# Performance work log

Measured on AMD Instinct MI355X. Metric: run time of the kernel, lower is better.

Reference implementation:

```python
import jax, jax.numpy as jnp
import numpy as np

K = 3
STRIDE = 1
PAD = 1


def setup_inputs() -> dict:
    key = jax.random.key(0)
    k1, k2, k3 = jax.random.split(key, 3)
    N, C, H, W = 4, 256, 64, 64
    outC = 256
    x = jax.random.normal(k1, (N, C, H, W), dtype=jnp.float32)
    # offset/mask conv params (torch inits these to 0; small random makes the test nontrivial)
    conv_offset_w = jax.random.normal(k2, (3 * K * K, C, K, K), dtype=jnp.float32) * 0.01
    conv_offset_b = jnp.zeros((3 * K * K,), dtype=jnp.float32)
    # xavier-normal scale for dcn weight
    fan = C * K * K + outC * K * K
    dcn_weight = jax.random.normal(k3, (outC, C, K, K), dtype=jnp.float32) * np.float32(np.sqrt(2.0 / fan))
    return {"x": x, "conv_offset_w": conv_offset_w, "conv_offset_b": conv_offset_b, "dcn_weight": dcn_weight}


def _dcn(x, w_off, b_off, dcn_weight):
    k, s, p = K, STRIDE, PAD
    N, C, H, W = x.shape
    outC = dcn_weight.shape[0]
    KK = k * k
    # offset/mask prediction conv
    om = jax.lax.conv_general_dilated(
        x, w_off, (s, s), [(p, p), (p, p)],
        dimension_numbers=("NCHW", "OIHW", "NCHW")) + b_off[None, :, None, None]
    offset = om[:, : 2 * KK]
    mask = jax.nn.sigmoid(om[:, 2 * KK:])
    oH = (H + 2 * p - (k - 1)) // s
    oW = (W + 2 * p - (k - 1)) // s
    # pad with an extra row/col at bottom-right so floor+1 indexing is in-bounds (as in torch code)
    px = jnp.pad(x, ((0, 0), (0, 0), (p, p + 1), (p, p + 1)))
    px = jnp.transpose(px, (0, 2, 3, 1))  # (N, H+2p+1, W+2p+1, C)
    offset = jnp.transpose(offset, (0, 2, 3, 1)).reshape(N, oH, oW, KK, 2)  # (...,(y,x))
    mask = jnp.transpose(mask, (0, 2, 3, 1))  # (N, oH, oW, KK)
    base_y = jnp.arange(oH, dtype=jnp.float32) * s + p
    base_x = jnp.arange(oW, dtype=jnp.float32) * s + p
    half = (k - 1) // 2
    inner_y = jnp.repeat(jnp.arange(k, dtype=jnp.float32) - half, k)  # kernel-tap y offsets
    inner_x = jnp.tile(jnp.arange(k, dtype=jnp.float32) - half, k)   # kernel-tap x offsets
    pos_y = base_y[None, :, None, None] + inner_y[None, None, None, :] + offset[..., 0]
    pos_x = base_x[None, None, :, None] + inner_x[None, None, None, :] + offset[..., 1]
    pos_y = jnp.clip(pos_y, 0.0, H + 2 * p - 1.0)
    pos_x = jnp.clip(pos_x, 0.0, W + 2 * p - 1.0)
    y1 = jnp.floor(pos_y)
    x1 = jnp.floor(pos_x)
    y1i = y1.astype(jnp.int32)
    x1i = x1.astype(jnp.int32)
    nidx = jnp.arange(N)[:, None, None, None]
    # bilinear gathers: each (N, oH, oW, KK, C)
    v1 = px[nidx, y1i, x1i]
    v2 = px[nidx, y1i, x1i + 1]
    v3 = px[nidx, y1i + 1, x1i]
    v4 = px[nidx, y1i + 1, x1i + 1]
    lh = (pos_y - y1)[..., None]
    lw = (pos_x - x1)[..., None]
    hh = 1.0 - lh
    hw = 1.0 - lw
    value = hh * hw * v1 + hh * lw * v2 + lh * hw * v3 + lh * lw * v4
    value = value * mask[..., None]  # modulated
    w = dcn_weight.reshape(outC, C, KK)
    # sum over in_C and kernel taps -> NCHW output
    out = jnp.einsum("nhwkc,ock->nohw", value, w)
    return out


def reference(x, conv_offset_w, conv_offset_b, dcn_weight):
    return _dcn(x, conv_offset_w, conv_offset_b, dcn_weight)
```

## Files before the change

kernel.cpp:

```cpp
#include <hip/hip_runtime.h>
#include <type_traits>


typedef __bf16 bf16x8 __attribute__((ext_vector_type(8)));
typedef float  f32x4  __attribute__((ext_vector_type(4)));
typedef unsigned short ushort8 __attribute__((ext_vector_type(8)));
typedef unsigned int   uint4v  __attribute__((ext_vector_type(4)));

#define XBF_OFF   0u
#define WREP_OFF  8388608u
#define WMAIN_OFF 8536064u
#define OM_OFF    9715712u

#define LGKM0_BAR() do { __builtin_amdgcn_s_waitcnt(0xC07F); __builtin_amdgcn_s_barrier(); } while (0)

template <int N> using ic = std::integral_constant<int, N>;

__device__ __forceinline__ unsigned short f2bf(float f) {
  unsigned int u = __float_as_uint(f);
  u += 0x7fffu + ((u >> 16) & 1u);
  return (unsigned short)(u >> 16);
}
__device__ __forceinline__ float bf2f(unsigned short h) {
  return __uint_as_float(((unsigned int)h) << 16);
}

__global__ __launch_bounds__(256) void k_pre(const float* __restrict__ x,
                                             const float* __restrict__ w_off,
                                             const float* __restrict__ dcn_w,
                                             unsigned short* __restrict__ xbf,
                                             unsigned short* __restrict__ wrep,
                                             unsigned short* __restrict__ wmain) {
  __shared__ float tile[32][65];
  __shared__ unsigned short lsh[2304];
  int b = blockIdx.x;
  int t = threadIdx.x;
  if (b < 2048) {
    int n  = b >> 9;
    int cb = (b >> 6) & 7;
    int xb = b & 63;
    int xx  = t & 63;
    int cc0 = t >> 6;
#pragma unroll
    for (int j = 0; j < 8; ++j) {
      int cc = cc0 + j * 4;
      tile[cc][xx] = x[((size_t)(n * 256 + cb * 32 + cc) << 12) + xb * 64 + xx];
    }
    __syncthreads();
    int ccw = t & 31;
    int xw0 = t >> 5;
#pragma unroll
    for (int j = 0; j < 8; ++j) {
      int xw = xw0 + j * 8;
      xbf[((size_t)((n << 12) + xb * 64 + xw)) * 256 + cb * 32 + ccw] = f2bf(tile[ccw][xw]);
    }
  } else {
    int ocb = b - 2048;
    const float* src;
    unsigned short* dst;
    int oc;
    if (ocb < 32) { oc = ocb; src = w_off; dst = wrep; }
    else          { oc = ocb - 32; src = dcn_w; dst = wmain; }
    if (ocb < 32 && oc >= 27) {
#pragma unroll
      for (int j = 0; j < 9; ++j) dst[oc * 2304 + j * 256 + t] = 0;
      return;
    }
    const float* base = src + (size_t)oc * 2304;
#pragma unroll
    for (int j = 0; j < 9; ++j) lsh[j * 256 + t] = f2bf(base[t * 9 + j]);
    __syncthreads();
#pragma unroll
    for (int j = 0; j < 9; ++j) dst[oc * 2304 + j * 256 + t] = lsh[j * 256 + t];
  }
}

__global__ __launch_bounds__(1024) void k_offconv(const unsigned short* __restrict__ xbf,
                                                  const unsigned short* __restrict__ wrep,
                                                  const float* __restrict__ bias,
                                                  float* __restrict__ om) {
  __shared__ __align__(16) unsigned short SHa[4][64 * 64];
  __shared__ __align__(16) unsigned short SHb[4][32 * 64];
  int t = threadIdx.x;
  int wave = t >> 6, lane = t & 63;
  int grp = wave >> 2, wv = wave & 3;
  int tg = t & 255;
  int bm = ((blockIdx.x & 7) << 5) + (blockIdx.x >> 3);
  int n = bm >> 6, oy = bm & 63;

  unsigned short* As = SHa[grp];
  unsigned short* Bs = SHb[grp];

  int arow = tg >> 2, acc4 = tg & 3;
  int brow = tg >> 3, bch = tg & 7;

  f32x4 acc0 = {0.f, 0.f, 0.f, 0.f};
  f32x4 acc1 = {0.f, 0.f, 0.f, 0.f};

  ushort8 av[2][2]; ushort8 bv[2];
  auto prefetch = [&](int ktg, auto slotc) {
    constexpr int slot = decltype(slotc)::value;
    int kk = ktg >> 2;
    int c0 = (ktg & 3) * 64;
    int dy = kk / 3 - 1, dx = kk % 3 - 1;
    int yy = oy + dy, xxg = arow + dx;
    bool ok = ((unsigned)yy < 64u) && ((unsigned)xxg < 64u);
    const unsigned short* p = xbf + (size_t)(((n * 64 + yy) * 64 + xxg) * 256 + c0 + acc4 * 16);
#pragma unroll
    for (int g = 0; g < 2; ++g)
      av[slot][g] = ok ? *(const ushort8*)(p + g * 8) : (ushort8){0,0,0,0,0,0,0,0};
    bv[slot] = *(const ushort8*)(wrep + (size_t)brow * 2304 + ktg * 64 + bch * 8);
  };

  int k0 = grp * 9;
  prefetch(k0, ic<0>{});
  prefetch(k0 + 1, ic<1>{});
  int mr = lane & 15, q = lane >> 4;

  auto step = [&](int kt, auto slotc) {
    constexpr int slot = decltype(slotc)::value;
    LGKM0_BAR();
#pragma unroll
    for (int g = 0; g < 2; ++g) {
      int ch = (acc4 * 2 + g) ^ (arow & 7);
      *(ushort8*)&As[arow * 64 + ch * 8] = av[slot][g];
    }
    { int ch = bch ^ (brow & 7);
      *(ushort8*)&Bs[brow * 64 + ch * 8] = bv[slot]; }
    if (kt + 2 < 9) prefetch(k0 + kt + 2, slotc);
    LGKM0_BAR();
#pragma unroll
    for (int kh = 0; kh < 2; ++kh) {
      int coff = ((q + kh * 4) ^ (mr & 7)) * 8;
      bf16x8 a  = *(const bf16x8*)&As[(wv * 16 + mr) * 64 + coff];
      bf16x8 b0 = *(const bf16x8*)&Bs[mr * 64 + coff];
      bf16x8 b1 = *(const bf16x8*)&Bs[(16 + mr) * 64 + coff];
      acc0 = __builtin_amdgcn_mfma_f32_16x16x32_bf16(a, b0, acc0, 0, 0, 0);
      acc1 = __builtin_amdgcn_mfma_f32_16x16x32_bf16(a, b1, acc1, 0, 0, 0);
    }
  };
  for (int kp = 0; kp < 4; ++kp) {
    step(2 * kp, ic<0>{});
    step(2 * kp + 1, ic<1>{});
  }
  step(8, ic<0>{});

  float* scratch = (float*)&SHa[0][0];
  __syncthreads();
  if (grp > 0) {
#pragma unroll
    for (int nt = 0; nt < 2; ++nt) {
      f32x4 a = nt ? acc1 : acc0;
#pragma unroll
      for (int rg = 0; rg < 4; ++rg)
        scratch[(grp - 1) * 2048 + (wv * 16 + q * 4 + rg) * 32 + nt * 16 + mr] = a[rg];
    }
  }
  __syncthreads();
  if (grp == 0) {
    int r0 = bm * 64;
#pragma unroll
    for (int nt = 0; nt < 2; ++nt) {
      f32x4 a = nt ? acc1 : acc0;
      int oc = nt * 16 + mr;
      float bvl = (oc < 27) ? bias[oc] : 0.f;
#pragma unroll
      for (int rg = 0; rg < 4; ++rg) {
        int pl = wv * 16 + q * 4 + rg;
        float v = a[rg] + bvl + scratch[pl * 32 + oc] +
                  scratch[2048 + pl * 32 + oc] + scratch[4096 + pl * 32 + oc];
        if (oc >= 18 && oc < 27) v = 1.f / (1.f + __expf(-v));
        om[(r0 + pl) * 32 + oc] = v;
      }
    }
  }
}

__global__ __launch_bounds__(1024) void k_gemm_fused(const unsigned short* __restrict__ xbf,
                                                     const float* __restrict__ om,
                                                     const unsigned short* __restrict__ wB,
                                                     float* __restrict__ out) {
  __shared__ __align__(16) unsigned short Ab[3][128 * 64];
  __shared__ __align__(16) unsigned short Bb[3][128 * 64];
  int t = threadIdx.x;
  int wave = t >> 6, lane = t & 63;
  int wm = wave & 3, wn = wave >> 2;
  int bmx = ((blockIdx.x & 7) << 4) + (blockIdx.x >> 3);
  int r0 = bmx * 128, o0 = blockIdx.y * 128;

  int srow = t >> 3;
  int sch  = (t & 7) * 8;
  int r = r0 + srow;
  int n = r >> 12, yx = r & 4095, oy = yx >> 6, ox = yx & 63;
  const unsigned short* xb = xbf + (size_t)n * (4096 * 256);
  const float* omr = om + (size_t)r * 32;
  const unsigned short* Bg = wB + (size_t)(o0 + srow) * 2304 + sch;
  int wch = ((t & 7) ^ (srow & 7)) * 8;

  f32x4 acc[2][2];
#pragma unroll
  for (int mt = 0; mt < 2; ++mt)
#pragma unroll
    for (int nt = 0; nt < 2; ++nt) acc[mt][nt] = (f32x4){0.f, 0.f, 0.f, 0.f};

  float pv_y, pv_x, pv_m;
  float cw1, cw2, cw3, cw4;
  int a1, a2, a3, a4;
  float wbuf[2][4];

  auto loadom = [&](int kk) {
    pv_y = omr[2 * kk]; pv_x = omr[2 * kk + 1]; pv_m = omr[18 + kk];
  };
  auto params = [&](int kk) {
    float py = (float)(oy + kk / 3) + pv_y;
    float px = (float)(ox + kk % 3) + pv_x;
    float m = pv_m;
    py = fminf(fmaxf(py, 0.f), 65.f);
    px = fminf(fmaxf(px, 0.f), 65.f);
    float fy = floorf(py), fx = floorf(px);
    float ly = py - fy, lx = px - fx;
    float hy = 1.f - ly, hx = 1.f - lx;
    int iy = (int)fy, ix = (int)fx;
    bool yv0 = (iy >= 1) && (iy <= 64);
    bool yv1 = (iy <= 63);
    bool xv0 = (ix >= 1) && (ix <= 64);
    bool xv1 = (ix <= 63);
    int y0 = min(max(iy - 1, 0), 63);
    int y1 = min(iy, 63);
    int x0 = min(max(ix - 1, 0), 63);
    int x1 = min(ix, 63);
    cw1 = (yv0 && xv0) ? hy * hx * m : 0.f;
    cw2 = (yv0 && xv1) ? hy * lx * m : 0.f;
    cw3 = (yv1 && xv0) ? ly * hx * m : 0.f;
    cw4 = (yv1 && xv1) ? ly * lx * m : 0.f;
    a1 = ((y0 << 6) + x0) * 256;
    a2 = ((y0 << 6) + x1) * 256;
    a3 = ((y1 << 6) + x0) * 256;
    a4 = ((y1 << 6) + x1) * 256;
  };

  ushort8 g1[2], g2[2], g3[2], g4[2], bv[2];
  auto issueA = [&](int ktg, auto slotc) {
    constexpr int slot = decltype(slotc)::value;
    wbuf[slot][0] = cw1; wbuf[slot][1] = cw2; wbuf[slot][2] = cw3; wbuf[slot][3] = cw4;
    int c = (ktg & 3) * 64 + sch;
    g1[slot] = *(const ushort8*)(xb + a1 + c);
    g2[slot] = *(const ushort8*)(xb + a2 + c);
    g3[slot] = *(const ushort8*)(xb + a3 + c);
    g4[slot] = *(const ushort8*)(xb + a4 + c);
  };
  auto issueB = [&](int ktg, auto slotc) {
    constexpr int slot = decltype(slotc)::value;
    bv[slot] = *(const ushort8*)(Bg + ktg * 64);
  };

  loadom(0);
  params(0);
  loadom(1);
  issueA(0, ic<0>{}); issueB(0, ic<0>{});
  issueA(1, ic<1>{}); issueB(1, ic<1>{});

  int mr = lane & 15, q = lane >> 4;

  auto step = [&](int k, auto slotc, auto bufc) {
    constexpr int slot = decltype(slotc)::value;
    constexpr int buf  = decltype(bufc)::value;
    uint4v rs;
#pragma unroll
    for (int p = 0; p < 4; ++p) {
      float va = wbuf[slot][0] * bf2f(g1[slot][2 * p])     + wbuf[slot][1] * bf2f(g2[slot][2 * p]) +
                 wbuf[slot][2] * bf2f(g3[slot][2 * p])     + wbuf[slot][3] * bf2f(g4[slot][2 * p]);
      float vb = wbuf[slot][0] * bf2f(g1[slot][2 * p + 1]) + wbuf[slot][1] * bf2f(g2[slot][2 * p + 1]) +
                 wbuf[slot][2] * bf2f(g3[slot][2 * p + 1]) + wbuf[slot][3] * bf2f(g4[slot][2 * p + 1]);
      unsigned ua = __float_as_uint(va) + 0x8000u;
      unsigned ub = __float_as_uint(vb) + 0x8000u;
      rs[p] = __builtin_amdgcn_perm(ub, ua, 0x07060302u);
    }
    *(uint4v*)&Ab[buf][srow * 64 + wch] = rs;
    *(ushort8*)&Bb[buf][srow * 64 + wch] = bv[slot];
    if (k + 2 < 36) {
      if (((k + 2) & 3) == 0) {
        int kk = (k + 2) >> 2;
        params(kk);
        loadom(kk < 8 ? kk + 1 : 8);
      }
      issueA(k + 2, slotc);
      issueB(k + 2, slotc);
    }
    LGKM0_BAR();
#pragma unroll
    for (int kh = 0; kh < 2; ++kh) {
      int coff = ((q + kh * 4) ^ (mr & 7)) * 8;
      bf16x8 af[2], bfv[2];
#pragma unroll
      for (int mt = 0; mt < 2; ++mt)
        af[mt] = *(const bf16x8*)&Ab[buf][(wm * 32 + mt * 16 + mr) * 64 + coff];
#pragma unroll
      for (int nt = 0; nt < 2; ++nt)
        bfv[nt] = *(const bf16x8*)&Bb[buf][(wn * 32 + nt * 16 + mr) * 64 + coff];
#pragma unroll
      for (int mt = 0; mt < 2; ++mt)
#pragma unroll
        for (int nt = 0; nt < 2; ++nt)
          acc[mt][nt] = __builtin_amdgcn_mfma_f32_16x16x32_bf16(af[mt], bfv[nt], acc[mt][nt], 0, 0, 0);
    }
  };

  for (int kp = 0; kp < 6; ++kp) {
    int k = kp * 6;
    step(k + 0, ic<0>{}, ic<0>{});
    step(k + 1, ic<1>{}, ic<1>{});
    step(k + 2, ic<0>{}, ic<2>{});
    step(k + 3, ic<1>{}, ic<0>{});
    step(k + 4, ic<0>{}, ic<1>{});
    step(k + 5, ic<1>{}, ic<2>{});
  }

#pragma unroll
  for (int mt = 0; mt < 2; ++mt)
#pragma unroll
    for (int nt = 0; nt < 2; ++nt) {
      int p = r0 + wm * 32 + mt * 16 + q * 4;
      int o = o0 + wn * 32 + nt * 16 + mr;
      int nn = p >> 12, pyx = p & 4095;
      *(f32x4*)(out + ((size_t)(nn * 256 + o) << 12) + pyx) = acc[mt][nt];
    }
}

extern "C" void kernel_launch(void* const* d_in, const int* in_sizes, int n_in,
                              void* d_out, int out_size, void* d_ws, size_t ws_size,
                              hipStream_t stream) {
  const float* x     = (const float*)d_in[0];
  const float* w_off = (const float*)d_in[1];
  const float* b_off = (const float*)d_in[2];
  const float* dcn_w = (const float*)d_in[3];
  float* out = (float*)d_out;
  char* ws = (char*)d_ws;
  unsigned short* xbf   = (unsigned short*)(ws + XBF_OFF);
  unsigned short* wrep  = (unsigned short*)(ws + WREP_OFF);
  unsigned short* wmain = (unsigned short*)(ws + WMAIN_OFF);
  float*          om    = (float*)(ws + OM_OFF);

  k_pre<<<2048 + 288, 256, 0, stream>>>(x, w_off, dcn_w, xbf, wrep, wmain);
  k_offconv<<<256, 1024, 0, stream>>>(xbf, wrep, b_off, om);
  k_gemm_fused<<<dim3(128, 2), 1024, 0, stream>>>(xbf, om, wmain, out);
}
```

Measured before the change: 131.5 us.

## Retile fused DCN GEMM to 64 rows by all 256 outputs with register-held weights

The fused sampling GEMM now has each block own 64 output pixels and all 256 output channels, instead of 128 pixels by 128 channels split over two grid columns. Bilinear sampling of each pixel is therefore done once rather than twice. Only half the threads sample into a double-buffered LDS A tile, while weight fragments are loaded straight from global memory into registers, which removes the B LDS staging. The pre-pass transpose also drops its LDS tile and has each thread convert 8 channels into one 16-byte store. The risks are idle threads during sampling, more register pressure and more global traffic for weights.

```diff
diff --git a/kernel.cpp b/kernel.cpp
--- a/kernel.cpp
+++ b/kernel.cpp
@@ -31,29 +31,25 @@
                                              unsigned short* __restrict__ xbf,
                                              unsigned short* __restrict__ wrep,
                                              unsigned short* __restrict__ wmain) {
-  __shared__ float tile[32][65];
   __shared__ unsigned short lsh[2304];
   int b = blockIdx.x;
   int t = threadIdx.x;
   if (b < 2048) {
     int n  = b >> 9;
-    int cb = (b >> 6) & 7;
-    int xb = b & 63;
-    int xx  = t & 63;
-    int cc0 = t >> 6;
-#pragma unroll
-    for (int j = 0; j < 8; ++j) {
-      int cc = cc0 + j * 4;
-      tile[cc][xx] = x[((size_t)(n * 256 + cb * 32 + cc) << 12) + xb * 64 + xx];
-    }
-    __syncthreads();
-    int ccw = t & 31;
-    int xw0 = t >> 5;
-#pragma unroll
-    for (int j = 0; j < 8; ++j) {
-      int xw = xw0 + j * 8;
-      xbf[((size_t)((n << 12) + xb * 64 + xw)) * 256 + cb * 32 + ccw] = f2bf(tile[ccw][xw]);
-    }
+    int cq = (b >> 4) & 31;
+    int yx = (b & 15) * 256 + t;
+    const float* xp = x + ((size_t)(n * 256 + cq * 8) << 12) + yx;
+    float v[8];
+#pragma unroll
+    for (int j = 0; j < 8; ++j) v[j] = xp[(size_t)j << 12];
+    uint4v rs;
+#pragma unroll
+    for (int p = 0; p < 4; ++p) {
+      unsigned ua = __float_as_uint(v[2 * p])     + 0x8000u;
+      unsigned ub = __float_as_uint(v[2 * p + 1]) + 0x8000u;
+      rs[p] = __builtin_amdgcn_perm(ub, ua, 0x07060302u);
+    }
+    *(uint4v*)(xbf + ((size_t)((n << 12) + yx)) * 256 + cq * 8) = rs;
   } else {
     int ocb = b - 2048;
     const float* src;
@@ -180,22 +176,25 @@
                                                      const float* __restrict__ om,
                                                      const unsigned short* __restrict__ wB,
                                                      float* __restrict__ out) {
-  __shared__ __align__(16) unsigned short Ab[3][128 * 64];
-  __shared__ __align__(16) unsigned short Bb[3][128 * 64];
+  __shared__ __align__(16) unsigned short Ab[2][64 * 64];
   int t = threadIdx.x;
   int wave = t >> 6, lane = t & 63;
-  int wm = wave & 3, wn = wave >> 2;
-  int bmx = ((blockIdx.x & 7) << 4) + (blockIdx.x >> 3);
-  int r0 = bmx * 128, o0 = blockIdx.y * 128;
-
+  int wm = wave & 1, wn = wave >> 1;
+  int bmx = ((blockIdx.x & 7) << 5) + (blockIdx.x >> 3);
+  int r0 = bmx * 64;
+
+  int mr = lane & 15, q = lane >> 4;
+  bool sampler = (t < 512);
   int srow = t >> 3;
   int sch  = (t & 7) * 8;
-  int r = r0 + srow;
+  int r = r0 + (sampler ? srow : 0);
   int n = r >> 12, yx = r & 4095, oy = yx >> 6, ox = yx & 63;
   const unsigned short* xb = xbf + (size_t)n * (4096 * 256);
   const float* omr = om + (size_t)r * 32;
-  const unsigned short* Bg = wB + (size_t)(o0 + srow) * 2304 + sch;
   int wch = ((t & 7) ^ (srow & 7)) * 8;
+
+  const unsigned short* Bl0 = wB + (size_t)(wn * 32 + mr) * 2304 + q * 8;
+  const unsigned short* Bl1 = Bl0 + (size_t)16 * 2304;
 
   f32x4 acc[2][2];
 #pragma unroll
@@ -239,81 +238,79 @@
     a4 = ((y1 << 6) + x1) * 256;
   };
 
-  ushort8 g1[2], g2[2], g3[2], g4[2], bv[2];
-  auto issueA = [&](int ktg, auto slotc) {
+  ushort8 g1[2], g2[2], g3[2], g4[2];
+  bf16x8 bfr[2][2][2];
+  auto issueA = [&](int k, auto slotc) {
     constexpr int slot = decltype(slotc)::value;
     wbuf[slot][0] = cw1; wbuf[slot][1] = cw2; wbuf[slot][2] = cw3; wbuf[slot][3] = cw4;
-    int c = (ktg & 3) * 64 + sch;
+    int c = (k & 3) * 64 + sch;
     g1[slot] = *(const ushort8*)(xb + a1 + c);
     g2[slot] = *(const ushort8*)(xb + a2 + c);
     g3[slot] = *(const ushort8*)(xb + a3 + c);
     g4[slot] = *(const ushort8*)(xb + a4 + c);
   };
-  auto issueB = [&](int ktg, auto slotc) {
-    constexpr int slot = decltype(slotc)::value;
-    bv[slot] = *(const ushort8*)(Bg + ktg * 64);
-  };
-
-  loadom(0);
-  params(0);
-  loadom(1);
-  issueA(0, ic<0>{}); issueB(0, ic<0>{});
-  issueA(1, ic<1>{}); issueB(1, ic<1>{});
-
-  int mr = lane & 15, q = lane >> 4;
-
-  auto step = [&](int k, auto slotc, auto bufc) {
-    constexpr int slot = decltype(slotc)::value;
-    constexpr int buf  = decltype(bufc)::value;
-    uint4v rs;
-#pragma unroll
-    for (int p = 0; p < 4; ++p) {
-      float va = wbuf[slot][0] * bf2f(g1[slot][2 * p])     + wbuf[slot][1] * bf2f(g2[slot][2 * p]) +
-                 wbuf[slot][2] * bf2f(g3[slot][2 * p])     + wbuf[slot][3] * bf2f(g4[slot][2 * p]);
-      float vb = wbuf[slot][0] * bf2f(g1[slot][2 * p + 1]) + wbuf[slot][1] * bf2f(g2[slot][2 * p + 1]) +
-                 wbuf[slot][2] * bf2f(g3[slot][2 * p + 1]) + wbuf[slot][3] * bf2f(g4[slot][2 * p + 1]);
-      unsigned ua = __float_as_uint(va) + 0x8000u;
-      unsigned ub = __float_as_uint(vb) + 0x8000u;
-      rs[p] = __builtin_amdgcn_perm(ub, ua, 0x07060302u);
-    }
-    *(uint4v*)&Ab[buf][srow * 64 + wch] = rs;
-    *(ushort8*)&Bb[buf][srow * 64 + wch] = bv[slot];
-    if (k + 2 < 36) {
-      if (((k + 2) & 3) == 0) {
-        int kk = (k + 2) >> 2;
-        params(kk);
-        loadom(kk < 8 ? kk + 1 : 8);
+  auto issueB = [&](int k, auto slotc) {
+    constexpr int slot = decltype(slotc)::value;
+#pragma unroll
+    for (int kh = 0; kh < 2; ++kh) {
+      bfr[slot][0][kh] = *(const bf16x8*)(Bl0 + k * 64 + kh * 32);
+      bfr[slot][1][kh] = *(const bf16x8*)(Bl1 + k * 64 + kh * 32);
+    }
+  };
+
+  if (sampler) {
+    loadom(0);
+    params(0);
+    loadom(1);
+    issueA(0, ic<0>{});
+    issueA(1, ic<1>{});
+  }
+  issueB(0, ic<0>{});
+
+  auto step = [&](int k, auto slotc) {
+    constexpr int slot = decltype(slotc)::value;
+    if (sampler) {
+      uint4v rs;
+#pragma unroll
+      for (int p = 0; p < 4; ++p) {
+        float va = wbuf[slot][0] * bf2f(g1[slot][2 * p])     + wbuf[slot][1] * bf2f(g2[slot][2 * p]) +
+                   wbuf[slot][2] * bf2f(g3[slot][2 * p])     + wbuf[slot][3] * bf2f(g4[slot][2 * p]);
+        float vb = wbuf[slot][0] * bf2f(g1[slot][2 * p + 1]) + wbuf[slot][1] * bf2f(g2[slot][2 * p + 1]) +
+                   wbuf[slot][2] * bf2f(g3[slot][2 * p + 1]) + wbuf[slot][3] * bf2f(g4[slot][2 * p + 1]);
+        unsigned ua = __float_as_uint(va) + 0x8000u;
+        unsigned ub = __float_as_uint(vb) + 0x8000u;
+        rs[p] = __builtin_amdgcn_perm(ub, ua, 0x07060302u);
       }
-      issueA(k + 2, slotc);
-      issueB(k + 2, slotc);
-    }
+      *(uint4v*)&Ab[slot][srow * 64 + wch] = rs;
+      if (k + 2 < 36) {
+        if (((k + 2) & 3) == 0) {
+          int kk = (k + 2) >> 2;
+          params(kk);
+          loadom(kk < 8 ? kk + 1 : 8);
+        }
+        issueA(k + 2, slotc);
+      }
+    }
+    if (k + 1 < 36) issueB(k + 1, ic<slot ^ 1>{});
     LGKM0_BAR();
 #pragma unroll
     for (int kh = 0; kh < 2; ++kh) {
       int coff = ((q + kh * 4) ^ (mr & 7)) * 8;
-      bf16x8 af[2], bfv[2];
+      bf16x8 af[2];
 #pragma unroll
       for (int mt = 0; mt < 2; ++mt)
-        af[mt] = *(const bf16x8*)&Ab[buf][(wm * 32 + mt * 16 + mr) * 64 + coff];
-#pragma unroll
-      for (int nt = 0; nt < 2; ++nt)
-        bfv[nt] = *(const bf16x8*)&Bb[buf][(wn * 32 + nt * 16 + mr) * 64 + coff];
+        af[mt] = *(const bf16x8*)&Ab[slot][(wm * 32 + mt * 16 + mr) * 64 + coff];
 #pragma unroll
       for (int mt = 0; mt < 2; ++mt)
 #pragma unroll
         for (int nt = 0; nt < 2; ++nt)
-          acc[mt][nt] = __builtin_amdgcn_mfma_f32_16x16x32_bf16(af[mt], bfv[nt], acc[mt][nt], 0, 0, 0);
-    }
-  };
-
-  for (int kp = 0; kp < 6; ++kp) {
-    int k = kp * 6;
-    step(k + 0, ic<0>{}, ic<0>{});
-    step(k + 1, ic<1>{}, ic<1>{});
-    step(k + 2, ic<0>{}, ic<2>{});
-    step(k + 3, ic<1>{}, ic<0>{});
-    step(k + 4, ic<0>{}, ic<1>{});
-    step(k + 5, ic<1>{}, ic<2>{});
+          acc[mt][nt] = __builtin_amdgcn_mfma_f32_16x16x32_bf16(af[mt], bfr[slot][nt][kh], acc[mt][nt], 0, 0, 0);
+    }
+  };
+
+  for (int kp = 0; kp < 18; ++kp) {
+    step(2 * kp, ic<0>{});
+    step(2 * kp + 1, ic<1>{});
   }
 
 #pragma unroll
@@ -321,7 +318,7 @@
 #pragma unroll
     for (int nt = 0; nt < 2; ++nt) {
       int p = r0 + wm * 32 + mt * 16 + q * 4;
-      int o = o0 + wn * 32 + nt * 16 + mr;
+      int o = wn * 32 + nt * 16 + mr;
       int nn = p >> 12, pyx = p & 4095;
       *(f32x4*)(out + ((size_t)(nn * 256 + o) << 12) + pyx) = acc[mt][nt];
     }
@@ -343,5 +340,5 @@
 
   k_pre<<<2048 + 288, 256, 0, stream>>>(x, w_off, dcn_w, xbf, wrep, wmain);
   k_offconv<<<256, 1024, 0, stream>>>(xbf, wrep, b_off, om);
-  k_gemm_fused<<<dim3(128, 2), 1024, 0, stream>>>(xbf, om, wmain, out);
-}
+  k_gemm_fused<<<256, 1024, 0, stream>>>(xbf, om, wmain, out);
+}
```

Measured after the change: 164.4 us. 24.9% more time.
